# Optimization experiments

Measured on AMD Instinct MI355X. Metric: run time of the kernel, lower is better.

## Reference

```python
import jax, jax.numpy as jnp
from jax import lax
import numpy as np

B, Z, Y, X = 2, 41, 400, 352   # KITTI-like sparse grid
N_TOTAL = 400000               # total active voxels (all batches)
C = 16                         # 16 * SCALING_RATIO channels in stage 1
K = 27                         # 3x3x3 kernel offsets
BN_EPS = 1e-3


def _build_rulebook(rng):
    """Random unique active voxels + [27,N] submanifold neighbor table (-1 = missing)."""
    per_b = N_TOTAL // B
    coords = []
    for b in range(B):
        flat = rng.choice(Z * Y * X, size=per_b, replace=False)
        z, r = np.divmod(flat, Y * X)
        y, x = np.divmod(r, X)
        coords.append(np.stack([np.full(per_b, b), z, y, x], axis=1))
    coords = np.concatenate(coords, 0).astype(np.int32)  # [N,4]
    # padded dense lookup: grid coord -> global voxel row, -1 if inactive
    lut = np.full((B, Z + 2, Y + 2, X + 2), -1, dtype=np.int32)
    lut[coords[:, 0], coords[:, 1] + 1, coords[:, 2] + 1, coords[:, 3] + 1] = np.arange(N_TOTAL, dtype=np.int32)
    offs = [(dz, dy, dx) for dz in (-1, 0, 1) for dy in (-1, 0, 1) for dx in (-1, 0, 1)]
    nbr = np.empty((K, N_TOTAL), dtype=np.int32)
    for k, (dz, dy, dx) in enumerate(offs):
        nbr[k] = lut[coords[:, 0], coords[:, 1] + 1 + dz, coords[:, 2] + 1 + dy, coords[:, 3] + 1 + dx]
    return nbr


def setup_inputs() -> dict:
    key = jax.random.key(0)
    kf, kw0, kw1, kg = jax.random.split(key, 4)
    rng = np.random.default_rng(0)
    nbr = jnp.asarray(_build_rulebook(rng))                      # [27, N] int32
    voxel_features = jax.random.normal(kf, (N_TOTAL, C), jnp.float32)
    w_in = jax.random.normal(kw0, (K, C, C), jnp.float32) * 0.05  # conv_input weight
    g_in = jnp.ones((C,), jnp.float32)
    b_in = jnp.zeros((C,), jnp.float32)
    # 2 SparseBasicBlocks x 2 convs each
    wb = jax.random.normal(kw1, (2, 2, K, C, C), jnp.float32) * 0.05
    gs = jnp.ones((2, 2, C), jnp.float32)
    bs = jnp.zeros((2, 2, C), jnp.float32)
    return {"voxel_features": voxel_features, "nbr": nbr, "w_in": w_in,
            "g_in": g_in, "b_in": b_in, "wb": wb, "gs": gs, "bs": bs}


def _subm_conv(feats, nbr, W):
    """Submanifold 3x3x3 conv: gather active neighbors, GEMM per offset, accumulate.
    feats [N,Cin], nbr [27,N] int32 (-1 = inactive), W [27,Cin,Cout] -> [N,Cout]."""
    out0 = jnp.zeros((feats.shape[0], W.shape[-1]), feats.dtype)
    def body(acc, kw):
        idx, Wk = kw
        valid = idx >= 0
        g = jnp.where(valid[:, None], feats[jnp.where(valid, idx, 0)], 0.0)
        return acc + g @ Wk, None
    acc, _ = lax.scan(body, out0, (nbr, W))
    return acc


def _bn(x, gamma, beta):
    # train-mode BatchNorm1d over voxel dim (biased var, eps=1e-3)
    m = x.mean(0)
    v = x.var(0)
    return (x - m) * lax.rsqrt(v + BN_EPS) * gamma + beta


def reference(voxel_features, nbr, w_in, g_in, b_in, wb, gs, bs):
    # conv_input: SubMConv3d -> BN -> ReLU
    x = jax.nn.relu(_bn(_subm_conv(voxel_features, nbr, w_in), g_in, b_in))
    # conv1: two SparseBasicBlocks sharing the 'subm1' rulebook
    for i in range(2):
        identity = x
        o = jax.nn.relu(_bn(_subm_conv(x, nbr, wb[i, 0]), gs[i, 0], bs[i, 0]))
        o = _bn(_subm_conv(o, nbr, wb[i, 1]), gs[i, 1], bs[i, 1])
        x = jax.nn.relu(o + identity)
    return x
```

## Files before the change

### kernel.cpp

```cpp
#include <hip/hip_runtime.h>

#define N_TOT  400000
#define NTILE  25000
#define NELEM  (N_TOT * 16)
#define CBLK   512
#define GS     (CBLK * 4)

typedef __attribute__((ext_vector_type(8))) short short8;
typedef __attribute__((ext_vector_type(4))) float f32x4;
typedef __attribute__((ext_vector_type(4))) unsigned short us4;

__device__ __forceinline__ unsigned short f2bf(float x) {
    unsigned int u = __float_as_uint(x);
    u += 0x7FFFu + ((u >> 16) & 1u);
    return (unsigned short)(u >> 16);
}
__device__ __forceinline__ float bf2f(unsigned short h) {
    return __uint_as_float(((unsigned int)h) << 16);
}

__global__ __launch_bounds__(64) void wfrag_k(const float* __restrict__ w_in,
                                              const float* __restrict__ wbs,
                                              unsigned short* __restrict__ wfrag,
                                              unsigned short* __restrict__ xb,
                                              unsigned short* __restrict__ ob) {
    if (blockIdx.x == 0 && threadIdx.x < 8) {
        us4 z = {0, 0, 0, 0};
        unsigned short* base = (threadIdx.x < 4) ? xb : ob;
        reinterpret_cast<us4*>(base + NELEM)[threadIdx.x & 3] = z;
    }
    int b = blockIdx.x;
    int L = b / 14, p = b % 14;
    int l = threadIdx.x;
    int g = l >> 4, col = l & 15;
    int k = 2 * p + (g >> 1);
    int cib = (g & 1) * 8;
    unsigned short v[8];
#pragma unroll
    for (int j = 0; j < 8; ++j) {
        float w = 0.f;
        if (k < 27) {
            int ci = cib + j;
            w = (L == 0) ? w_in[(k * 16 + ci) * 16 + col]
                         : wbs[(((L - 1) * 27 + k) * 16 + ci) * 16 + col];
        }
        v[j] = f2bf(w);
    }
    unsigned short* dst = wfrag + (size_t)(b * 64 + l) * 8;
#pragma unroll
    for (int j = 0; j < 8; ++j) dst[j] = v[j];
}

__global__ __launch_bounds__(256) void cvt_k(const float* __restrict__ in,
                                             unsigned short* __restrict__ out) {
    int i = (blockIdx.x * 256 + threadIdx.x) * 8;
    f32x4 a = *reinterpret_cast<const f32x4*>(in + i);
    f32x4 b = *reinterpret_cast<const f32x4*>(in + i + 4);
    short8 o = { (short)f2bf(a[0]), (short)f2bf(a[1]), (short)f2bf(a[2]), (short)f2bf(a[3]),
                 (short)f2bf(b[0]), (short)f2bf(b[1]), (short)f2bf(b[2]), (short)f2bf(b[3]) };
    *reinterpret_cast<short8*>(out + i) = o;
}

#define IDX(I, tt)                                                              \
  {                                                                             \
    const int vv = (tt) * 16;                                                   \
    _Pragma("unroll")                                                           \
    for (int p = 0; p < 14; ++p) {                                              \
      int k = 2 * p + ksel;                                                     \
      if (k == 13)      I[p] = vv + rc;                                         \
      else if (k < 27)  I[p] = nbr[(size_t)k * N_TOT + vv + rc];                \
      else              I[p] = -1;                                              \
    }                                                                           \
  }

#define GAT(A, I)                                                               \
  {                                                                             \
    _Pragma("unroll")                                                           \
    for (int p = 0; p < 14; ++p) {                                              \
      int ci = I[p] < 0 ? N_TOT : I[p];                                         \
      A[p] = *reinterpret_cast<const short8*>(feats + ((size_t)ci << 4) + half);\
    }                                                                           \
  }

#define CMP(A, tt)                                                              \
  {                                                                             \
    f32x4 ac0 = {0.f, 0.f, 0.f, 0.f};                                           \
    f32x4 ac1 = {0.f, 0.f, 0.f, 0.f};                                           \
    _Pragma("unroll")                                                           \
    for (int p = 0; p < 14; p += 2) {                                           \
      ac0 = __builtin_amdgcn_mfma_f32_16x16x32_bf16(A[p],     B[p],     ac0, 0, 0, 0); \
      ac1 = __builtin_amdgcn_mfma_f32_16x16x32_bf16(A[p + 1], B[p + 1], ac1, 0, 0, 0); \
    }                                                                           \
    f32x4 acc = ac0 + ac1;                                                      \
    const int vv = (tt) * 16;                                                   \
    _Pragma("unroll")                                                           \
    for (int i = 0; i < 4; ++i)                                                 \
      raw[(size_t)(vv + g * 4 + i) * 16 + rc] = f2bf(acc[i]);                   \
    s_acc += acc[0] + acc[1] + acc[2] + acc[3];                                 \
    q_acc += acc[0]*acc[0] + acc[1]*acc[1] + acc[2]*acc[2] + acc[3]*acc[3];     \
  }

__global__ __launch_bounds__(256, 2) void conv_k(const unsigned short* __restrict__ feats,
                                                 const int* __restrict__ nbr,
                                                 const unsigned short* __restrict__ wfrag,
                                                 unsigned short* __restrict__ raw,
                                                 float* __restrict__ partials) {
    __shared__ float red[128];

    const int lane = threadIdx.x & 63;
    const int wv   = threadIdx.x >> 6;
    const int g    = lane >> 4;
    const int rc   = lane & 15;
    const int half = (g & 1) * 8;
    const int ksel = g >> 1;

    short8 B[14];
#pragma unroll
    for (int p = 0; p < 14; ++p)
        B[p] = *reinterpret_cast<const short8*>(wfrag + (size_t)(p * 64 + lane) * 8);

    float s_acc = 0.f, q_acc = 0.f;

    int I0[14], I1[14];
    short8 A0[14], A1[14];

    int t0 = blockIdx.x * 4 + wv;
    IDX(I0, t0);
    GAT(A0, I0);
    int t1 = t0 + GS;
    if (t1 < NTILE) IDX(I1, t1);

    for (;;) {
        int t2 = t0 + 2 * GS;
        if (t2 < NTILE) IDX(I0, t2);
        if (t1 < NTILE) GAT(A1, I1);
        __builtin_amdgcn_sched_barrier(0);
        CMP(A0, t0);
        if (t1 >= NTILE) break;

        int t3 = t1 + 2 * GS;
        if (t3 < NTILE) IDX(I1, t3);
        if (t2 < NTILE) GAT(A0, I0);
        __builtin_amdgcn_sched_barrier(0);
        CMP(A1, t1);
        if (t2 >= NTILE) break;

        t0 = t2;
        t1 = t2 + GS;
    }

    s_acc += __shfl_xor(s_acc, 16);  s_acc += __shfl_xor(s_acc, 32);
    q_acc += __shfl_xor(q_acc, 16);  q_acc += __shfl_xor(q_acc, 32);
    if (lane < 16) {
        red[wv * 32 + rc]      = s_acc;
        red[wv * 32 + 16 + rc] = q_acc;
    }
    __syncthreads();
    if (threadIdx.x < 32) {
        float v = red[threadIdx.x] + red[32 + threadIdx.x] +
                  red[64 + threadIdx.x] + red[96 + threadIdx.x];
        partials[(size_t)threadIdx.x * CBLK + blockIdx.x] = v;
    }
}

__global__ __launch_bounds__(256) void reduce_k(const float* __restrict__ partials,
                                                float* __restrict__ S) {
    int c = blockIdx.x;
    float s = 0.f;
    for (int i = threadIdx.x; i < CBLK; i += 256) s += partials[(size_t)c * CBLK + i];
    __shared__ float red[256];
    red[threadIdx.x] = s;
    __syncthreads();
#pragma unroll
    for (int off = 128; off > 0; off >>= 1) {
        if (threadIdx.x < off) red[threadIdx.x] += red[threadIdx.x + off];
        __syncthreads();
    }
    if (threadIdx.x == 0) S[c] = red[0];
}

__global__ __launch_bounds__(256) void apply_k(const unsigned short* __restrict__ raw,
                                               const float* __restrict__ S,
                                               const float* __restrict__ gamma,
                                               const float* __restrict__ beta,
                                               const unsigned short* residb,
                                               unsigned short* bfout,
                                               float* f32out) {
    int i = (blockIdx.x * 256 + threadIdx.x) * 8;
    int c0 = i & 8;
    short8 r8 = *reinterpret_cast<const short8*>(raw + i);
    float res[8] = {0, 0, 0, 0, 0, 0, 0, 0};
    if (residb) {
        short8 x8 = *reinterpret_cast<const short8*>(residb + i);
#pragma unroll
        for (int j = 0; j < 8; ++j) res[j] = bf2f((unsigned short)x8[j]);
    }
    const float inv = 1.0f / (float)N_TOT;
    float val[8];
#pragma unroll
    for (int j = 0; j < 8; ++j) {
        int c = c0 + j;
        float m   = S[c] * inv;
        float var = S[16 + c] * inv - m * m;
        float sc  = gamma[c] * rsqrtf(var + 1e-3f);
        float sh  = beta[c] - m * sc;
        val[j] = fmaxf(bf2f((unsigned short)r8[j]) * sc + sh + res[j], 0.f);
    }
    if (bfout) {
        short8 o = { (short)f2bf(val[0]), (short)f2bf(val[1]), (short)f2bf(val[2]), (short)f2bf(val[3]),
                     (short)f2bf(val[4]), (short)f2bf(val[5]), (short)f2bf(val[6]), (short)f2bf(val[7]) };
        *reinterpret_cast<short8*>(bfout + i) = o;
    }
    if (f32out) {
        f32x4 lo = { val[0], val[1], val[2], val[3] };
        f32x4 hi = { val[4], val[5], val[6], val[7] };
        *reinterpret_cast<f32x4*>(f32out + i)     = lo;
        *reinterpret_cast<f32x4*>(f32out + i + 4) = hi;
    }
}

extern "C" void kernel_launch(void* const* d_in, const int* in_sizes, int n_in,
                              void* d_out, int out_size, void* d_ws, size_t ws_size,
                              hipStream_t stream) {
    const float* vf   = (const float*)d_in[0];
    const int*   nbr  = (const int*)  d_in[1];
    const float* w_in = (const float*)d_in[2];
    const float* g_in = (const float*)d_in[3];
    const float* b_in = (const float*)d_in[4];
    const float* wbs  = (const float*)d_in[5];
    const float* gs   = (const float*)d_in[6];
    const float* bs   = (const float*)d_in[7];
    float* out = (float*)d_out;

    char* ws = (char*)d_ws;
    size_t off = 0;
    auto alloc = [&](size_t b) { char* p = ws + off; off += (b + 255) & ~(size_t)255; return p; };
    unsigned short* wfrag = (unsigned short*)alloc((size_t)5 * 14 * 64 * 8 * 2);
    unsigned short* xb    = (unsigned short*)alloc((size_t)(NELEM + 16) * 2);
    unsigned short* ob    = (unsigned short*)alloc((size_t)(NELEM + 16) * 2);
    unsigned short* rb    = (unsigned short*)alloc((size_t)NELEM * 2);
    float*          part  = (float*)alloc((size_t)32 * CBLK * 4);
    float*          S     = (float*)alloc(32 * 4);

    const int FR = 14 * 64 * 8;

    wfrag_k<<<70, 64, 0, stream>>>(w_in, wbs, wfrag, xb, ob);
    cvt_k<<<3125, 256, 0, stream>>>(vf, xb);

    conv_k<<<CBLK, 256, 0, stream>>>(xb, nbr, wfrag, rb, part);
    reduce_k<<<32, 256, 0, stream>>>(part, S);
    apply_k<<<3125, 256, 0, stream>>>(rb, S, g_in, b_in, nullptr, xb, nullptr);

    conv_k<<<CBLK, 256, 0, stream>>>(xb, nbr, wfrag + FR, rb, part);
    reduce_k<<<32, 256, 0, stream>>>(part, S);
    apply_k<<<3125, 256, 0, stream>>>(rb, S, gs + 0, bs + 0, nullptr, ob, nullptr);

    conv_k<<<CBLK, 256, 0, stream>>>(ob, nbr, wfrag + 2 * FR, rb, part);
    reduce_k<<<32, 256, 0, stream>>>(part, S);
    apply_k<<<3125, 256, 0, stream>>>(rb, S, gs + 16, bs + 16, xb, xb, nullptr);

    conv_k<<<CBLK, 256, 0, stream>>>(xb, nbr, wfrag + 3 * FR, rb, part);
    reduce_k<<<32, 256, 0, stream>>>(part, S);
    apply_k<<<3125, 256, 0, stream>>>(rb, S, gs + 32, bs + 32, nullptr, ob, nullptr);

    conv_k<<<CBLK, 256, 0, stream>>>(ob, nbr, wfrag + 4 * FR, rb, part);
    reduce_k<<<32, 256, 0, stream>>>(part, S);
    apply_k<<<3125, 256, 0, stream>>>(rb, S, gs + 48, bs + 48, xb, nullptr, out);
}
```

Baseline: 175.5 us.

## Prepack neighbor indices per tile and transpose MFMA output for vector stores

Adds a pack kernel that rearranges the neighbor table into per-lane contiguous 16-int records, so each conv lane loads its indices with four 16-byte loads instead of fourteen strided scalar loads. It also swaps the MFMA A/B operands so each lane holds four channels of one voxel, allowing a single 8-byte packed store of the bf16 result and per-channel stat accumulation with a different shuffle reduction. The cost is an extra packing pass and a padded index buffer that is larger than the original table, read by every conv.

```diff
diff --git a/kernel.cpp b/kernel.cpp
--- a/kernel.cpp
+++ b/kernel.cpp
@@ -9,6 +9,7 @@
 typedef __attribute__((ext_vector_type(8))) short short8;
 typedef __attribute__((ext_vector_type(4))) float f32x4;
 typedef __attribute__((ext_vector_type(4))) unsigned short us4;
+typedef __attribute__((ext_vector_type(4))) int i32x4;
 
 __device__ __forceinline__ unsigned short f2bf(float x) {
     unsigned int u = __float_as_uint(x);
@@ -51,6 +52,30 @@
     for (int j = 0; j < 8; ++j) dst[j] = v[j];
 }
 
+__global__ __launch_bounds__(256) void pack_k(const int* __restrict__ nbr,
+                                              int* __restrict__ idxpk) {
+    int wid  = (blockIdx.x * 256 + threadIdx.x) >> 6;
+    int lane = threadIdx.x & 63;
+    int t    = wid * 2 + (lane >> 5);
+    int j    = lane & 31;
+    int ksel = j >> 4, rc = j & 15;
+    int v = t * 16 + rc;
+    int I[16];
+#pragma unroll
+    for (int p = 0; p < 14; ++p) {
+        int k = 2 * p + ksel;
+        if (k == 13)      I[p] = v;
+        else if (k < 27)  I[p] = nbr[(size_t)k * N_TOT + v];
+        else              I[p] = -1;
+    }
+    I[14] = -1; I[15] = -1;
+    int* dst = idxpk + ((size_t)t * 32 + j) * 16;
+#pragma unroll
+    for (int q = 0; q < 4; ++q)
+        *reinterpret_cast<i32x4*>(dst + q * 4) =
+            *reinterpret_cast<const i32x4*>(&I[q * 4]);
+}
+
 __global__ __launch_bounds__(256) void cvt_k(const float* __restrict__ in,
                                              unsigned short* __restrict__ out) {
     int i = (blockIdx.x * 256 + threadIdx.x) * 8;
@@ -63,14 +88,11 @@
 
 #define IDX(I, tt)                                                              \
   {                                                                             \
-    const int vv = (tt) * 16;                                                   \
+    const int* bp = idxpk + ((size_t)(tt) * 32 + jrow) * 16;                    \
     _Pragma("unroll")                                                           \
-    for (int p = 0; p < 14; ++p) {                                              \
-      int k = 2 * p + ksel;                                                     \
-      if (k == 13)      I[p] = vv + rc;                                         \
-      else if (k < 27)  I[p] = nbr[(size_t)k * N_TOT + vv + rc];                \
-      else              I[p] = -1;                                              \
-    }                                                                           \
+    for (int q = 0; q < 4; ++q)                                                 \
+      *reinterpret_cast<i32x4*>(&I[q * 4]) =                                    \
+          *reinterpret_cast<const i32x4*>(bp + q * 4);                          \
   }
 
 #define GAT(A, I)                                                               \
@@ -88,20 +110,22 @@
     f32x4 ac1 = {0.f, 0.f, 0.f, 0.f};                                           \
     _Pragma("unroll")                                                           \
     for (int p = 0; p < 14; p += 2) {                                           \
-      ac0 = __builtin_amdgcn_mfma_f32_16x16x32_bf16(A[p],     B[p],     ac0, 0, 0, 0); \
-      ac1 = __builtin_amdgcn_mfma_f32_16x16x32_bf16(A[p + 1], B[p + 1], ac1, 0, 0, 0); \
+      ac0 = __builtin_amdgcn_mfma_f32_16x16x32_bf16(W[p],     A[p],     ac0, 0, 0, 0); \
+      ac1 = __builtin_amdgcn_mfma_f32_16x16x32_bf16(W[p + 1], A[p + 1], ac1, 0, 0, 0); \
     }                                                                           \
     f32x4 acc = ac0 + ac1;                                                      \
     const int vv = (tt) * 16;                                                   \
+    us4 pk = { f2bf(acc[0]), f2bf(acc[1]), f2bf(acc[2]), f2bf(acc[3]) };        \
+    *reinterpret_cast<us4*>(raw + ((size_t)(vv + rc) * 16 + hi * 4)) = pk;      \
     _Pragma("unroll")                                                           \
-    for (int i = 0; i < 4; ++i)                                                 \
-      raw[(size_t)(vv + g * 4 + i) * 16 + rc] = f2bf(acc[i]);                   \
-    s_acc += acc[0] + acc[1] + acc[2] + acc[3];                                 \
-    q_acc += acc[0]*acc[0] + acc[1]*acc[1] + acc[2]*acc[2] + acc[3]*acc[3];     \
+    for (int i = 0; i < 4; ++i) {                                               \
+      s_acc[i] += acc[i];                                                       \
+      q_acc[i] += acc[i] * acc[i];                                              \
+    }                                                                           \
   }
 
 __global__ __launch_bounds__(256, 2) void conv_k(const unsigned short* __restrict__ feats,
-                                                 const int* __restrict__ nbr,
+                                                 const int* __restrict__ idxpk,
                                                  const unsigned short* __restrict__ wfrag,
                                                  unsigned short* __restrict__ raw,
                                                  float* __restrict__ partials) {
@@ -109,19 +133,21 @@
 
     const int lane = threadIdx.x & 63;
     const int wv   = threadIdx.x >> 6;
-    const int g    = lane >> 4;
+    const int hi   = lane >> 4;
     const int rc   = lane & 15;
-    const int half = (g & 1) * 8;
-    const int ksel = g >> 1;
-
-    short8 B[14];
+    const int half = (hi & 1) * 8;
+    const int ksel = hi >> 1;
+    const int jrow = ksel * 16 + rc;
+
+    short8 W[14];
 #pragma unroll
     for (int p = 0; p < 14; ++p)
-        B[p] = *reinterpret_cast<const short8*>(wfrag + (size_t)(p * 64 + lane) * 8);
-
-    float s_acc = 0.f, q_acc = 0.f;
-
-    int I0[14], I1[14];
+        W[p] = *reinterpret_cast<const short8*>(wfrag + (size_t)(p * 64 + lane) * 8);
+
+    float s_acc[4] = {0.f, 0.f, 0.f, 0.f};
+    float q_acc[4] = {0.f, 0.f, 0.f, 0.f};
+
+    int I0[16], I1[16];
     short8 A0[14], A1[14];
 
     int t0 = blockIdx.x * 4 + wv;
@@ -149,11 +175,19 @@
         t1 = t2 + GS;
     }
 
-    s_acc += __shfl_xor(s_acc, 16);  s_acc += __shfl_xor(s_acc, 32);
-    q_acc += __shfl_xor(q_acc, 16);  q_acc += __shfl_xor(q_acc, 32);
-    if (lane < 16) {
-        red[wv * 32 + rc]      = s_acc;
-        red[wv * 32 + 16 + rc] = q_acc;
+#pragma unroll
+    for (int i = 0; i < 4; ++i) {
+        s_acc[i] += __shfl_xor(s_acc[i], 1);  s_acc[i] += __shfl_xor(s_acc[i], 2);
+        s_acc[i] += __shfl_xor(s_acc[i], 4);  s_acc[i] += __shfl_xor(s_acc[i], 8);
+        q_acc[i] += __shfl_xor(q_acc[i], 1);  q_acc[i] += __shfl_xor(q_acc[i], 2);
+        q_acc[i] += __shfl_xor(q_acc[i], 4);  q_acc[i] += __shfl_xor(q_acc[i], 8);
+    }
+    if (rc == 0) {
+#pragma unroll
+        for (int i = 0; i < 4; ++i) {
+            red[wv * 32 + hi * 4 + i]      = s_acc[i];
+            red[wv * 32 + 16 + hi * 4 + i] = q_acc[i];
+        }
     }
     __syncthreads();
     if (threadIdx.x < 32) {
@@ -239,31 +273,33 @@
     unsigned short* xb    = (unsigned short*)alloc((size_t)(NELEM + 16) * 2);
     unsigned short* ob    = (unsigned short*)alloc((size_t)(NELEM + 16) * 2);
     unsigned short* rb    = (unsigned short*)alloc((size_t)NELEM * 2);
+    int*            idxpk = (int*)alloc((size_t)NTILE * 32 * 16 * 4);
     float*          part  = (float*)alloc((size_t)32 * CBLK * 4);
     float*          S     = (float*)alloc(32 * 4);
 
     const int FR = 14 * 64 * 8;
 
     wfrag_k<<<70, 64, 0, stream>>>(w_in, wbs, wfrag, xb, ob);
+    pack_k<<<3125, 256, 0, stream>>>(nbr, idxpk);
     cvt_k<<<3125, 256, 0, stream>>>(vf, xb);
 
-    conv_k<<<CBLK, 256, 0, stream>>>(xb, nbr, wfrag, rb, part);
+    conv_k<<<CBLK, 256, 0, stream>>>(xb, idxpk, wfrag, rb, part);
     reduce_k<<<32, 256, 0, stream>>>(part, S);
     apply_k<<<3125, 256, 0, stream>>>(rb, S, g_in, b_in, nullptr, xb, nullptr);
 
-    conv_k<<<CBLK, 256, 0, stream>>>(xb, nbr, wfrag + FR, rb, part);
+    conv_k<<<CBLK, 256, 0, stream>>>(xb, idxpk, wfrag + FR, rb, part);
     reduce_k<<<32, 256, 0, stream>>>(part, S);
     apply_k<<<3125, 256, 0, stream>>>(rb, S, gs + 0, bs + 0, nullptr, ob, nullptr);
 
-    conv_k<<<CBLK, 256, 0, stream>>>(ob, nbr, wfrag + 2 * FR, rb, part);
+    conv_k<<<CBLK, 256, 0, stream>>>(ob, idxpk, wfrag + 2 * FR, rb, part);
     reduce_k<<<32, 256, 0, stream>>>(part, S);
     apply_k<<<3125, 256, 0, stream>>>(rb, S, gs + 16, bs + 16, xb, xb, nullptr);
 
-    conv_k<<<CBLK, 256, 0, stream>>>(xb, nbr, wfrag + 3 * FR, rb, part);
+    conv_k<<<CBLK, 256, 0, stream>>>(xb, idxpk, wfrag + 3 * FR, rb, part);
     reduce_k<<<32, 256, 0, stream>>>(part, S);
     apply_k<<<3125, 256, 0, stream>>>(rb, S, gs + 32, bs + 32, nullptr, ob, nullptr);
 
-    conv_k<<<CBLK, 256, 0, stream>>>(ob, nbr, wfrag + 4 * FR, rb, part);
+    conv_k<<<CBLK, 256, 0, stream>>>(ob, idxpk, wfrag + 4 * FR, rb, part);
     reduce_k<<<32, 256, 0, stream>>>(part, S);
     apply_k<<<3125, 256, 0, stream>>>(rb, S, gs + 48, bs + 48, xb, nullptr, out);
 }
```

Result: slower. 200.5 us (+14.2%).

## Pack neighbor rulebook into per-tile compressed 19-bit index layout

Applied to the files above, without the earlier changes.

Adds a build kernel that repacks the [27,N] int32 neighbor table into per-16-voxel tiles holding 16-bit low indices plus 3-bit high parts packed into 64-bit words, with missing neighbors mapped to the zero row. The five conv passes read this compact, contiguous block instead of 27 strided int32 rows, which reduces index bandwidth and removes the per-entry validity select. The weight-fragment and feature-conversion kernels are also merged into a single prep launch. The trade-off is an extra repacking pass and workspace, plus a few extra bit operations per gather.

```diff
diff --git a/kernel.cpp b/kernel.cpp
--- a/kernel.cpp
+++ b/kernel.cpp
@@ -5,6 +5,7 @@
 #define NELEM  (N_TOT * 16)
 #define CBLK   512
 #define GS     (CBLK * 4)
+#define PKB    1152
 
 typedef __attribute__((ext_vector_type(8))) short short8;
 typedef __attribute__((ext_vector_type(4))) float f32x4;
@@ -19,65 +20,93 @@
     return __uint_as_float(((unsigned int)h) << 16);
 }
 
-__global__ __launch_bounds__(64) void wfrag_k(const float* __restrict__ w_in,
+__global__ __launch_bounds__(256) void build_k(const int* __restrict__ nbr,
+                                               char* __restrict__ pk) {
+    int gt = blockIdx.x * 256 + threadIdx.x;
+    if (gt >= N_TOT) return;
+    int t = gt >> 4, rc = gt & 15;
+    int v = gt;
+    char* bp = pk + (size_t)t * PKB;
+    unsigned long long hv0 = 0ull, hv1 = 0ull;
+#pragma unroll
+    for (int k = 0; k < 28; ++k) {
+        int id;
+        if (k == 13)      id = v;
+        else if (k == 27) id = N_TOT;
+        else {
+            int n = nbr[(size_t)k * N_TOT + v];
+            id = n < 0 ? N_TOT : n;
+        }
+        *reinterpret_cast<unsigned short*>(bp + k * 32 + rc * 2) =
+            (unsigned short)(id & 0xFFFF);
+        unsigned long long hi = (unsigned)(id >> 16);
+        int p = k >> 1;
+        if (k & 1) hv1 |= hi << (3 * p);
+        else       hv0 |= hi << (3 * p);
+    }
+    *reinterpret_cast<unsigned long long*>(bp + 896 + rc * 8)       = hv0;
+    *reinterpret_cast<unsigned long long*>(bp + 896 + 128 + rc * 8) = hv1;
+}
+
+__global__ __launch_bounds__(256) void prep_k(const float* __restrict__ vf,
+                                              const float* __restrict__ w_in,
                                               const float* __restrict__ wbs,
-                                              unsigned short* __restrict__ wfrag,
                                               unsigned short* __restrict__ xb,
-                                              unsigned short* __restrict__ ob) {
-    if (blockIdx.x == 0 && threadIdx.x < 8) {
-        us4 z = {0, 0, 0, 0};
-        unsigned short* base = (threadIdx.x < 4) ? xb : ob;
-        reinterpret_cast<us4*>(base + NELEM)[threadIdx.x & 3] = z;
-    }
+                                              unsigned short* __restrict__ ob,
+                                              unsigned short* __restrict__ wfrag) {
     int b = blockIdx.x;
-    int L = b / 14, p = b % 14;
-    int l = threadIdx.x;
-    int g = l >> 4, col = l & 15;
-    int k = 2 * p + (g >> 1);
-    int cib = (g & 1) * 8;
-    unsigned short v[8];
-#pragma unroll
-    for (int j = 0; j < 8; ++j) {
-        float w = 0.f;
-        if (k < 27) {
-            int ci = cib + j;
-            w = (L == 0) ? w_in[(k * 16 + ci) * 16 + col]
-                         : wbs[(((L - 1) * 27 + k) * 16 + ci) * 16 + col];
+    if (b < 3125) {
+        int i = (b * 256 + threadIdx.x) * 8;
+        f32x4 a = *reinterpret_cast<const f32x4*>(vf + i);
+        f32x4 c = *reinterpret_cast<const f32x4*>(vf + i + 4);
+        short8 o = { (short)f2bf(a[0]), (short)f2bf(a[1]), (short)f2bf(a[2]), (short)f2bf(a[3]),
+                     (short)f2bf(c[0]), (short)f2bf(c[1]), (short)f2bf(c[2]), (short)f2bf(c[3]) };
+        *reinterpret_cast<short8*>(xb + i) = o;
+    } else if (b < 3195) {
+        if (threadIdx.x >= 64) return;
+        int wb = b - 3125;
+        int L = wb / 14, p = wb % 14;
+        int l = threadIdx.x;
+        int g = l >> 4, col = l & 15;
+        int k = 2 * p + (g >> 1);
+        int cib = (g & 1) * 8;
+        unsigned short v[8];
+#pragma unroll
+        for (int j = 0; j < 8; ++j) {
+            float w = 0.f;
+            if (k < 27) {
+                int ci = cib + j;
+                w = (L == 0) ? w_in[(k * 16 + ci) * 16 + col]
+                             : wbs[(((L - 1) * 27 + k) * 16 + ci) * 16 + col];
+            }
+            v[j] = f2bf(w);
         }
-        v[j] = f2bf(w);
-    }
-    unsigned short* dst = wfrag + (size_t)(b * 64 + l) * 8;
-#pragma unroll
-    for (int j = 0; j < 8; ++j) dst[j] = v[j];
-}
-
-__global__ __launch_bounds__(256) void cvt_k(const float* __restrict__ in,
-                                             unsigned short* __restrict__ out) {
-    int i = (blockIdx.x * 256 + threadIdx.x) * 8;
-    f32x4 a = *reinterpret_cast<const f32x4*>(in + i);
-    f32x4 b = *reinterpret_cast<const f32x4*>(in + i + 4);
-    short8 o = { (short)f2bf(a[0]), (short)f2bf(a[1]), (short)f2bf(a[2]), (short)f2bf(a[3]),
-                 (short)f2bf(b[0]), (short)f2bf(b[1]), (short)f2bf(b[2]), (short)f2bf(b[3]) };
-    *reinterpret_cast<short8*>(out + i) = o;
-}
-
-#define IDX(I, tt)                                                              \
+        unsigned short* dst = wfrag + (size_t)(wb * 64 + l) * 8;
+#pragma unroll
+        for (int j = 0; j < 8; ++j) dst[j] = v[j];
+    } else {
+        if (threadIdx.x < 8) {
+            us4 z = {0, 0, 0, 0};
+            unsigned short* base = (threadIdx.x < 4) ? xb : ob;
+            reinterpret_cast<us4*>(base + NELEM)[threadIdx.x & 3] = z;
+        }
+    }
+}
+
+#define IDXP(L, HV, tt)                                                         \
   {                                                                             \
-    const int vv = (tt) * 16;                                                   \
+    const char* bp = pkc + (size_t)(tt) * PKB;                                  \
+    HV = *reinterpret_cast<const unsigned long long*>(bp + hvoff);              \
     _Pragma("unroll")                                                           \
-    for (int p = 0; p < 14; ++p) {                                              \
-      int k = 2 * p + ksel;                                                     \
-      if (k == 13)      I[p] = vv + rc;                                         \
-      else if (k < 27)  I[p] = nbr[(size_t)k * N_TOT + vv + rc];                \
-      else              I[p] = -1;                                              \
-    }                                                                           \
+    for (int p = 0; p < 14; ++p)                                                \
+      L[p] = *reinterpret_cast<const unsigned short*>(bp + (2 * p + ksel) * 32 + rc2); \
   }
 
-#define GAT(A, I)                                                               \
+#define GAT(A, L, HV)                                                           \
   {                                                                             \
     _Pragma("unroll")                                                           \
     for (int p = 0; p < 14; ++p) {                                              \
-      int ci = I[p] < 0 ? N_TOT : I[p];                                         \
+      int ci = (int)(L[p] | ((((unsigned)(HV >> (3 * p))) & 7u) << 16));        \
       A[p] = *reinterpret_cast<const short8*>(feats + ((size_t)ci << 4) + half);\
     }                                                                           \
   }
@@ -101,7 +130,7 @@
   }
 
 __global__ __launch_bounds__(256, 2) void conv_k(const unsigned short* __restrict__ feats,
-                                                 const int* __restrict__ nbr,
+                                                 const char* __restrict__ pkc,
                                                  const unsigned short* __restrict__ wfrag,
                                                  unsigned short* __restrict__ raw,
                                                  float* __restrict__ partials) {
@@ -113,6 +142,8 @@
     const int rc   = lane & 15;
     const int half = (g & 1) * 8;
     const int ksel = g >> 1;
+    const int rc2  = rc * 2;
+    const int hvoff = 896 + (ksel * 16 + rc) * 8;
 
     short8 B[14];
 #pragma unroll
@@ -121,26 +152,27 @@
 
     float s_acc = 0.f, q_acc = 0.f;
 
-    int I0[14], I1[14];
+    unsigned L0[14], L1[14];
+    unsigned long long HV0, HV1;
     short8 A0[14], A1[14];
 
     int t0 = blockIdx.x * 4 + wv;
-    IDX(I0, t0);
-    GAT(A0, I0);
+    IDXP(L0, HV0, t0);
+    GAT(A0, L0, HV0);
     int t1 = t0 + GS;
-    if (t1 < NTILE) IDX(I1, t1);
+    if (t1 < NTILE) IDXP(L1, HV1, t1);
 
     for (;;) {
         int t2 = t0 + 2 * GS;
-        if (t2 < NTILE) IDX(I0, t2);
-        if (t1 < NTILE) GAT(A1, I1);
+        if (t2 < NTILE) IDXP(L0, HV0, t2);
+        if (t1 < NTILE) GAT(A1, L1, HV1);
         __builtin_amdgcn_sched_barrier(0);
         CMP(A0, t0);
         if (t1 >= NTILE) break;
 
         int t3 = t1 + 2 * GS;
-        if (t3 < NTILE) IDX(I1, t3);
-        if (t2 < NTILE) GAT(A0, I0);
+        if (t3 < NTILE) IDXP(L1, HV1, t3);
+        if (t2 < NTILE) GAT(A0, L0, HV0);
         __builtin_amdgcn_sched_barrier(0);
         CMP(A1, t1);
         if (t2 >= NTILE) break;
@@ -239,31 +271,32 @@
     unsigned short* xb    = (unsigned short*)alloc((size_t)(NELEM + 16) * 2);
     unsigned short* ob    = (unsigned short*)alloc((size_t)(NELEM + 16) * 2);
     unsigned short* rb    = (unsigned short*)alloc((size_t)NELEM * 2);
+    char*           pk    = alloc((size_t)NTILE * PKB);
     float*          part  = (float*)alloc((size_t)32 * CBLK * 4);
     float*          S     = (float*)alloc(32 * 4);
 
     const int FR = 14 * 64 * 8;
 
-    wfrag_k<<<70, 64, 0, stream>>>(w_in, wbs, wfrag, xb, ob);
-    cvt_k<<<3125, 256, 0, stream>>>(vf, xb);
-
-    conv_k<<<CBLK, 256, 0, stream>>>(xb, nbr, wfrag, rb, part);
+    build_k<<<1563, 256, 0, stream>>>(nbr, pk);
+    prep_k<<<3196, 256, 0, stream>>>(vf, w_in, wbs, xb, ob, wfrag);
+
+    conv_k<<<CBLK, 256, 0, stream>>>(xb, pk, wfrag, rb, part);
     reduce_k<<<32, 256, 0, stream>>>(part, S);
     apply_k<<<3125, 256, 0, stream>>>(rb, S, g_in, b_in, nullptr, xb, nullptr);
 
-    conv_k<<<CBLK, 256, 0, stream>>>(xb, nbr, wfrag + FR, rb, part);
+    conv_k<<<CBLK, 256, 0, stream>>>(xb, pk, wfrag + FR, rb, part);
     reduce_k<<<32, 256, 0, stream>>>(part, S);
     apply_k<<<3125, 256, 0, stream>>>(rb, S, gs + 0, bs + 0, nullptr, ob, nullptr);
 
-    conv_k<<<CBLK, 256, 0, stream>>>(ob, nbr, wfrag + 2 * FR, rb, part);
+    conv_k<<<CBLK, 256, 0, stream>>>(ob, pk, wfrag + 2 * FR, rb, part);
     reduce_k<<<32, 256, 0, stream>>>(part, S);
     apply_k<<<3125, 256, 0, stream>>>(rb, S, gs + 16, bs + 16, xb, xb, nullptr);
 
-    conv_k<<<CBLK, 256, 0, stream>>>(xb, nbr, wfrag + 3 * FR, rb, part);
+    conv_k<<<CBLK, 256, 0, stream>>>(xb, pk, wfrag + 3 * FR, rb, part);
     reduce_k<<<32, 256, 0, stream>>>(part, S);
     apply_k<<<3125, 256, 0, stream>>>(rb, S, gs + 32, bs + 32, nullptr, ob, nullptr);
 
-    conv_k<<<CBLK, 256, 0, stream>>>(ob, nbr, wfrag + 4 * FR, rb, part);
+    conv_k<<<CBLK, 256, 0, stream>>>(ob, pk, wfrag + 4 * FR, rb, part);
     reduce_k<<<32, 256, 0, stream>>>(part, S);
     apply_k<<<3125, 256, 0, stream>>>(rb, S, gs + 48, bs + 48, xb, nullptr, out);
 }
```

After: 181.4 us. 1.03x slower.
